# Kernel optimization log

Measured on AMD Instinct MI355X. Metric: run time of the kernel, lower is better.

The kernel has to match this reference:

```python
import jax, jax.numpy as jnp
import numpy as np

N = 100000
E = 1600000
IN_F, HID, OUT_F = 256, 128, 64


def setup_inputs() -> dict:
    key = jax.random.key(0)
    k_x, k_e, k_w1, k_w2, k_b1, k_b2 = jax.random.split(key, 6)
    x = jax.random.normal(k_x, (N, IN_F), dtype=jnp.float32)
    edge_index = jax.random.randint(k_e, (2, E), 0, N, dtype=jnp.int32)
    # GCNConv params: lin has no bias in PyG; separate additive bias per layer.
    W1 = jax.random.normal(k_w1, (IN_F, HID), dtype=jnp.float32) / np.sqrt(IN_F)
    b1 = jax.random.normal(k_b1, (HID,), dtype=jnp.float32) * 0.01
    W2 = jax.random.normal(k_w2, (HID, OUT_F), dtype=jnp.float32) / np.sqrt(HID)
    b2 = jax.random.normal(k_b2, (OUT_F,), dtype=jnp.float32) * 0.01
    return {"x": x, "edge_index": edge_index, "W1": W1, "b1": b1, "W2": W2, "b2": b2}


def _gcn_norm(edge_index, num_nodes):
    # add self loops (improved=False -> weight 1.0), symmetric normalization
    loop = jnp.arange(num_nodes, dtype=edge_index.dtype)
    src = jnp.concatenate([edge_index[0], loop])
    dst = jnp.concatenate([edge_index[1], loop])
    w = jnp.ones(src.shape[0], dtype=jnp.float32)
    deg = jax.ops.segment_sum(w, dst, num_segments=num_nodes)
    dinv = jnp.where(deg > 0, jax.lax.rsqrt(deg), 0.0)
    norm = dinv[src] * w * dinv[dst]
    return src, dst, norm


def _gcn_layer(h, W, b, src, dst, norm, num_nodes):
    h = h @ W                               # [N, out]
    msg = h[src] * norm[:, None]            # [E+N, out] gather + scale
    out = jax.ops.segment_sum(msg, dst, num_segments=num_nodes)  # scatter-add
    return out + b


def reference(x, edge_index, W1, b1, W2, b2):
    # dropout is identity in eval mode
    src, dst, norm = _gcn_norm(edge_index, N)
    h = _gcn_layer(x, W1, b1, src, dst, norm, N)
    h = jax.nn.relu(h)
    out = _gcn_layer(h, W2, b2, src, dst, norm, N)
    return out
```

## Files before the change

### kernel.cpp

```cpp
#include <hip/hip_runtime.h>
#include <hip/hip_bf16.h>

#define N_NODES 100000
#define N_EDGES 1600000
#define IN_FEAT 256
#define HID_F   128
#define OUT_FT  64

#define NBUK   256
#define NPB    391
#define BUKCAP 8192
#define EPB    4096
#define G_BIN  ((N_EDGES + EPB - 1) / EPB)
#define G_GEMM ((N_NODES + 127) / 128)
#define G_CAST ((IN_FEAT * HID_F + HID_F * OUT_FT + 255) / 256)
#define G_AGG  ((N_NODES + 7) / 8)

typedef unsigned short u16;
typedef __attribute__((ext_vector_type(8))) unsigned short u16x8;
typedef __attribute__((ext_vector_type(8))) short short8;
typedef __attribute__((ext_vector_type(4))) float f32x4;

static __device__ inline u16 f2bf(float f) {
    __hip_bfloat16 h = __float2bfloat16(f);
    return *reinterpret_cast<u16*>(&h);
}
static __device__ inline float bf2f(u16 u) {
    union { unsigned u; float f; } c;
    c.u = ((unsigned)u) << 16;
    return c.f;
}


__global__ __launch_bounds__(256) void k_bin(const int* __restrict__ srcA,
                                             const int* __restrict__ dstA,
                                             int* __restrict__ gcur, int2* __restrict__ pairs,
                                             const float* __restrict__ W1,
                                             const float* __restrict__ W2,
                                             u16* __restrict__ W1t, u16* __restrict__ W2t) {
    if (blockIdx.x >= G_BIN) {
        int idx = (blockIdx.x - G_BIN) * 256 + threadIdx.x;
        if (idx < IN_FEAT * HID_F) {
            int k = idx / HID_F, n = idx % HID_F;
            W1t[n * IN_FEAT + k] = f2bf(W1[idx]);
        } else {
            int e2 = idx - IN_FEAT * HID_F;
            if (e2 < HID_F * OUT_FT) {
                int k = e2 / OUT_FT, n = e2 % OUT_FT;
                W2t[n * HID_F + k] = f2bf(W2[e2]);
            }
        }
        return;
    }
    __shared__ int lh[NBUK];
    int t = threadIdx.x;
    int e0 = blockIdx.x * EPB;
    if (t < NBUK) lh[t] = 0;
    __syncthreads();
#pragma unroll
    for (int i = 0; i < EPB / 256; i++) {
        int e = e0 + i * 256 + t;
        if (e < N_EDGES) atomicAdd(&lh[dstA[e] / NPB], 1);
    }
    __syncthreads();
    if (t < NBUK) {
        int c = lh[t];
        lh[t] = atomicAdd(&gcur[t], c);
    }
    __syncthreads();
#pragma unroll
    for (int i = 0; i < EPB / 256; i++) {
        int e = e0 + i * 256 + t;
        if (e < N_EDGES) {
            int d = dstA[e];
            int b = d / NPB;
            int p = atomicAdd(&lh[b], 1);
            if (p < BUKCAP) pairs[(size_t)b * BUKCAP + p] = make_int2(srcA[e], d);
        }
    }
}


__global__ __launch_bounds__(256) void k_fillB(const int2* __restrict__ pairs,
                                               const int* __restrict__ gcnt,
                                               int* __restrict__ offsets,
                                               float* __restrict__ dinv,
                                               int* __restrict__ csr) {
    __shared__ int hist[NPB];
    __shared__ int sm[256];
    __shared__ int s_ebase;
    int b = blockIdx.x, t = threadIdx.x;
    int nbase = b * NPB;
    int nn = min(NPB, N_NODES - nbase);

    int gv = gcnt[t];
    sm[t] = gv;
    __syncthreads();
    for (int o = 1; o < 256; o <<= 1) {
        int u = (t >= o) ? sm[t - o] : 0;
        __syncthreads();
        sm[t] += u;
        __syncthreads();
    }
    if (t == b) s_ebase = sm[t] - gv;
    __syncthreads();
    int ebase = s_ebase;
    int cnt = gcnt[b];
    const int2* pb = pairs + (size_t)b * BUKCAP;

    for (int i = t; i < NPB; i += 256) hist[i] = 0;
    __syncthreads();
    for (int i = t; i < cnt; i += 256) atomicAdd(&hist[pb[i].y - nbase], 1);
    __syncthreads();

    int base2 = t * 2;
    int c0 = (base2 < NPB) ? hist[base2] : 0;
    int c1 = (base2 + 1 < NPB) ? hist[base2 + 1] : 0;
    int s = c0 + c1;
    __syncthreads();
    sm[t] = s;
    __syncthreads();
    for (int o = 1; o < 256; o <<= 1) {
        int u = (t >= o) ? sm[t - o] : 0;
        __syncthreads();
        sm[t] += u;
        __syncthreads();
    }
    int run = ebase + sm[t] - s;
    __syncthreads();
    int cc[2] = {c0, c1};
#pragma unroll
    for (int q = 0; q < 2; q++) {
        int n = base2 + q;
        if (n < nn) {
            int g = nbase + n;
            offsets[g] = run;
            dinv[g] = rsqrtf((float)(cc[q] + 1));
            hist[n] = run;
            run += cc[q];
        }
    }
    __syncthreads();
    for (int i = t; i < cnt; i += 256) {
        int2 e = pb[i];
        int p = atomicAdd(&hist[e.y - nbase], 1);
        csr[p] = e.x;
    }
    if (b == NBUK - 1 && t == 0) offsets[N_NODES] = N_EDGES;
}


__global__ __launch_bounds__(256) void k_gemm1(const float* __restrict__ A,
                                               const u16* __restrict__ Bt,
                                               const float* __restrict__ dinv,
                                               u16* __restrict__ C) {
    __shared__ u16 As[128][40];
    __shared__ u16 Bs[128][40];
    int tid = threadIdx.x;
    int wv = tid >> 6, lane = tid & 63;
    int m16 = lane & 15, quad = lane >> 4;
    int row0 = blockIdx.x * 128;
    int r = tid >> 1, h = tid & 1;
    int grow_s = row0 + r;
    bool rok = grow_s < N_NODES;

    f32x4 acc[2][8];
#pragma unroll
    for (int i = 0; i < 2; i++)
#pragma unroll
        for (int j = 0; j < 8; j++) acc[i][j] = (f32x4)(0.f);

    for (int k0 = 0; k0 < IN_FEAT; k0 += 32) {
        f32x4 v0 = (f32x4)(0.f), v1 = v0, v2 = v0, v3 = v0;
        if (rok) {
            const f32x4* src = (const f32x4*)&A[(size_t)grow_s * IN_FEAT + k0 + h * 16];
            v0 = src[0]; v1 = src[1]; v2 = src[2]; v3 = src[3];
        }
        u16x8 p0, p1;
#pragma unroll
        for (int j = 0; j < 4; j++) {
            p0[j] = f2bf(v0[j]); p0[4 + j] = f2bf(v1[j]);
            p1[j] = f2bf(v2[j]); p1[4 + j] = f2bf(v3[j]);
        }
        *(u16x8*)&As[r][h * 16] = p0;
        *(u16x8*)&As[r][h * 16 + 8] = p1;
        const u16x8* bsrc = (const u16x8*)&Bt[(size_t)r * IN_FEAT + k0 + h * 16];
        *(u16x8*)&Bs[r][h * 16] = bsrc[0];
        *(u16x8*)&Bs[r][h * 16 + 8] = bsrc[1];
        __syncthreads();

        short8 af0 = *(const short8*)&As[32 * wv + m16][quad * 8];
        short8 af1 = *(const short8*)&As[32 * wv + 16 + m16][quad * 8];
#pragma unroll
        for (int ct = 0; ct < 8; ct++) {
            short8 bf = *(const short8*)&Bs[16 * ct + m16][quad * 8];
            acc[0][ct] = __builtin_amdgcn_mfma_f32_16x16x32_bf16(af0, bf, acc[0][ct], 0, 0, 0);
            acc[1][ct] = __builtin_amdgcn_mfma_f32_16x16x32_bf16(af1, bf, acc[1][ct], 0, 0, 0);
        }
        __syncthreads();
    }
#pragma unroll
    for (int rt = 0; rt < 2; rt++)
#pragma unroll
        for (int r4 = 0; r4 < 4; r4++) {
            int grow = row0 + 32 * wv + 16 * rt + quad * 4 + r4;
            if (grow < N_NODES) {
                float dv = dinv[grow];
#pragma unroll
                for (int ct = 0; ct < 8; ct++)
                    C[(size_t)grow * HID_F + 16 * ct + m16] = f2bf(acc[rt][ct][r4] * dv);
            }
        }
}


__global__ __launch_bounds__(256) void k_gemm2(const u16* __restrict__ A,
                                               const u16* __restrict__ Bt,
                                               const float* __restrict__ dinv,
                                               u16* __restrict__ C) {
    __shared__ u16 As[128][40];
    __shared__ u16 Bs[64][40];
    int tid = threadIdx.x;
    int wv = tid >> 6, lane = tid & 63;
    int m16 = lane & 15, quad = lane >> 4;
    int row0 = blockIdx.x * 128;
    int r = tid >> 1, h = tid & 1;
    int grow_s = row0 + r;
    bool rok = grow_s < N_NODES;
    int nb = tid >> 2, q = tid & 3;

    f32x4 acc[2][4];
#pragma unroll
    for (int i = 0; i < 2; i++)
#pragma unroll
        for (int j = 0; j < 4; j++) acc[i][j] = (f32x4)(0.f);

    for (int k0 = 0; k0 < HID_F; k0 += 32) {
        u16x8 a0 = (u16x8)(0), a1v = (u16x8)(0);
        if (rok) {
            const u16x8* src = (const u16x8*)&A[(size_t)grow_s * HID_F + k0 + h * 16];
            a0 = src[0]; a1v = src[1];
        }
        *(u16x8*)&As[r][h * 16] = a0;
        *(u16x8*)&As[r][h * 16 + 8] = a1v;
        *(u16x8*)&Bs[nb][q * 8] = *(const u16x8*)&Bt[(size_t)nb * HID_F + k0 + q * 8];
        __syncthreads();

        short8 af0 = *(const short8*)&As[32 * wv + m16][quad * 8];
        short8 af1 = *(const short8*)&As[32 * wv + 16 + m16][quad * 8];
#pragma unroll
        for (int ct = 0; ct < 4; ct++) {
            short8 bf = *(const short8*)&Bs[16 * ct + m16][quad * 8];
            acc[0][ct] = __builtin_amdgcn_mfma_f32_16x16x32_bf16(af0, bf, acc[0][ct], 0, 0, 0);
            acc[1][ct] = __builtin_amdgcn_mfma_f32_16x16x32_bf16(af1, bf, acc[1][ct], 0, 0, 0);
        }
        __syncthreads();
    }
#pragma unroll
    for (int rt = 0; rt < 2; rt++)
#pragma unroll
        for (int r4 = 0; r4 < 4; r4++) {
            int grow = row0 + 32 * wv + 16 * rt + quad * 4 + r4;
            if (grow < N_NODES) {
                float dv = dinv[grow];
#pragma unroll
                for (int ct = 0; ct < 4; ct++)
                    C[(size_t)grow * OUT_FT + 16 * ct + m16] = f2bf(acc[rt][ct][r4] * dv);
            }
        }
}


__global__ __launch_bounds__(256) void k_agg1(const u16* __restrict__ hs,
                                              const int* __restrict__ offsets,
                                              const int* __restrict__ csr,
                                              const float* __restrict__ dinv,
                                              const float* __restrict__ b,
                                              u16* __restrict__ out) {
    int wave = threadIdx.x >> 6;
    int lane = threadIdx.x & 63;
    int half = lane >> 5;
    int node = blockIdx.x * 8 + wave * 2 + half;
    if (node >= N_NODES) return;
    int gl = lane & 31;
    int g = gl >> 4;
    int fl = gl & 15;
    const int fo = fl * 8;
    int beg = offsets[node], end = offsets[node + 1];

    float accA[8], accB[8];
#pragma unroll
    for (int i = 0; i < 8; i++) { accA[i] = 0.f; accB[i] = 0.f; }

    int j = beg;
    for (; j + 8 <= end; j += 8) {
        int s0 = csr[j + g];
        int s1 = csr[j + 2 + g];
        int s2 = csr[j + 4 + g];
        int s3 = csr[j + 6 + g];
        u16x8 r0 = *(const u16x8*)&hs[(size_t)s0 * HID_F + fo];
        u16x8 r1 = *(const u16x8*)&hs[(size_t)s1 * HID_F + fo];
        u16x8 r2 = *(const u16x8*)&hs[(size_t)s2 * HID_F + fo];
        u16x8 r3 = *(const u16x8*)&hs[(size_t)s3 * HID_F + fo];
#pragma unroll
        for (int i = 0; i < 8; i++) {
            accA[i] += bf2f(r0[i]) + bf2f(r1[i]);
            accB[i] += bf2f(r2[i]) + bf2f(r3[i]);
        }
    }
    if (j + 4 <= end) {
        int s0 = csr[j + g];
        int s1 = csr[j + 2 + g];
        u16x8 r0 = *(const u16x8*)&hs[(size_t)s0 * HID_F + fo];
        u16x8 r1 = *(const u16x8*)&hs[(size_t)s1 * HID_F + fo];
#pragma unroll
        for (int i = 0; i < 8; i++) accA[i] += bf2f(r0[i]) + bf2f(r1[i]);
        j += 4;
    }
    for (; j < end; j += 2) {
        int idx = j + g;
        if (idx < end) {
            int s = csr[idx];
            u16x8 r0 = *(const u16x8*)&hs[(size_t)s * HID_F + fo];
#pragma unroll
            for (int i = 0; i < 8; i++) accB[i] += bf2f(r0[i]);
        }
    }
#pragma unroll
    for (int i = 0; i < 8; i++) {
        float v = accA[i] + accB[i];
        v += __shfl_xor(v, 16, 64);
        accA[i] = v;
    }
    if (g == 0) {
        u16x8 sr = *(const u16x8*)&hs[(size_t)node * HID_F + fo];
        float dv = dinv[node];
        f32x4 b0 = *(const f32x4*)&b[fo];
        f32x4 b1 = *(const f32x4*)&b[fo + 4];
        u16x8 o;
#pragma unroll
        for (int i = 0; i < 4; i++) {
            o[i]     = f2bf(fmaxf(dv * (accA[i]     + bf2f(sr[i]))     + b0[i], 0.f));
            o[4 + i] = f2bf(fmaxf(dv * (accA[4 + i] + bf2f(sr[4 + i])) + b1[i], 0.f));
        }
        *(u16x8*)&out[(size_t)node * HID_F + fo] = o;
    }
}


__global__ __launch_bounds__(256) void k_agg2(const u16* __restrict__ hs,
                                              const int* __restrict__ offsets,
                                              const int* __restrict__ csr,
                                              const float* __restrict__ dinv,
                                              const float* __restrict__ b,
                                              float* __restrict__ out) {
    int wave = threadIdx.x >> 6;
    int lane = threadIdx.x & 63;
    int half = lane >> 5;
    int node = blockIdx.x * 8 + wave * 2 + half;
    if (node >= N_NODES) return;
    int gl = lane & 31;
    int g = gl >> 3;
    int fl = gl & 7;
    const int fo = fl * 8;
    int beg = offsets[node], end = offsets[node + 1];

    float accA[8], accB[8];
#pragma unroll
    for (int i = 0; i < 8; i++) { accA[i] = 0.f; accB[i] = 0.f; }

    int j = beg;
    for (; j + 16 <= end; j += 16) {
        int s0 = csr[j + g];
        int s1 = csr[j + 4 + g];
        int s2 = csr[j + 8 + g];
        int s3 = csr[j + 12 + g];
        u16x8 r0 = *(const u16x8*)&hs[(size_t)s0 * OUT_FT + fo];
        u16x8 r1 = *(const u16x8*)&hs[(size_t)s1 * OUT_FT + fo];
        u16x8 r2 = *(const u16x8*)&hs[(size_t)s2 * OUT_FT + fo];
        u16x8 r3 = *(const u16x8*)&hs[(size_t)s3 * OUT_FT + fo];
#pragma unroll
        for (int i = 0; i < 8; i++) {
            accA[i] += bf2f(r0[i]) + bf2f(r1[i]);
            accB[i] += bf2f(r2[i]) + bf2f(r3[i]);
        }
    }
    if (j + 8 <= end) {
        int s0 = csr[j + g];
        int s1 = csr[j + 4 + g];
        u16x8 r0 = *(const u16x8*)&hs[(size_t)s0 * OUT_FT + fo];
        u16x8 r1 = *(const u16x8*)&hs[(size_t)s1 * OUT_FT + fo];
#pragma unroll
        for (int i = 0; i < 8; i++) accA[i] += bf2f(r0[i]) + bf2f(r1[i]);
        j += 8;
    }
    for (; j < end; j += 4) {
        int idx = j + g;
        if (idx < end) {
            int s = csr[idx];
            u16x8 r0 = *(const u16x8*)&hs[(size_t)s * OUT_FT + fo];
#pragma unroll
            for (int i = 0; i < 8; i++) accB[i] += bf2f(r0[i]);
        }
    }
#pragma unroll
    for (int i = 0; i < 8; i++) {
        float v = accA[i] + accB[i];
        v += __shfl_xor(v, 8, 64);
        v += __shfl_xor(v, 16, 64);
        accA[i] = v;
    }
    if (g == 0) {
        u16x8 sr = *(const u16x8*)&hs[(size_t)node * OUT_FT + fo];
        float dv = dinv[node];
        f32x4 b0 = *(const f32x4*)&b[fo];
        f32x4 b1 = *(const f32x4*)&b[fo + 4];
        f32x4 o0, o1;
#pragma unroll
        for (int i = 0; i < 4; i++) {
            o0[i] = dv * (accA[i]     + bf2f(sr[i]))     + b0[i];
            o1[i] = dv * (accA[4 + i] + bf2f(sr[4 + i])) + b1[i];
        }
        *(f32x4*)&out[(size_t)node * OUT_FT + fo] = o0;
        *(f32x4*)&out[(size_t)node * OUT_FT + fo + 4] = o1;
    }
}


extern "C" void kernel_launch(void* const* d_in, const int* in_sizes, int n_in,
                              void* d_out, int out_size, void* d_ws, size_t ws_size,
                              hipStream_t stream) {
    const float* x  = (const float*)d_in[0];
    const int*   ei = (const int*)d_in[1];
    const float* W1 = (const float*)d_in[2];
    const float* b1 = (const float*)d_in[3];
    const float* W2 = (const float*)d_in[4];
    const float* b2 = (const float*)d_in[5];
    float* out = (float*)d_out;

    char* ws = (char*)d_ws;
    int*   offsets = (int*)(ws + 0);
    float* dinv    = (float*)(ws + 400512);
    int*   csr     = (int*)(ws + 800512);
    u16*   W1t     = (u16*)(ws + 7200512);
    u16*   W2t     = (u16*)(ws + 7266048);
    int*   gcur    = (int*)(ws + 7282432);
    u16*   hs1     = (u16*)(ws + 7284608);
    u16*   a1      = (u16*)(ws + 32884608);
    int2*  pairs   = (int2*)(ws + 32884608);
    u16*   hs2     = hs1;

    const int* srcA = ei;
    const int* dstA = ei + N_EDGES;

    hipMemsetAsync(gcur, 0, NBUK * sizeof(int), stream);

    k_bin<<<G_BIN + G_CAST, 256, 0, stream>>>(srcA, dstA, gcur, pairs, W1, W2, W1t, W2t);
    k_fillB<<<NBUK, 256, 0, stream>>>(pairs, gcur, offsets, dinv, csr);

    k_gemm1<<<G_GEMM, 256, 0, stream>>>(x, W1t, dinv, hs1);
    k_agg1<<<G_AGG, 256, 0, stream>>>(hs1, offsets, csr, dinv, b1, a1);
    k_gemm2<<<G_GEMM, 256, 0, stream>>>(a1, W2t, dinv, hs2);
    k_agg2<<<G_AGG, 256, 0, stream>>>(hs2, offsets, csr, dinv, b2, out);
}
```

Measured before the change: 345.1 us.

## Drop LDS staging in GEMM kernels, load MFMA fragments directly from global

Both dense projection kernels stop staging A and B tiles through shared memory and no longer synchronise the block. Each wave now loads its A fragment and the B fragments straight from global memory into registers. Each wave covers 16 rows instead of 32, so the row tile per block drops to 64 and the grid doubles. This removes LDS traffic and barrier stalls. In exchange, B is re-read from global/L2 by every wave and A loads are strided 32-byte chunks per lane rather than coalesced rows.

Result: slower. 382.6 us (+10.9%).

```diff
diff --git a/kernel.cpp b/kernel.cpp
--- a/kernel.cpp
+++ b/kernel.cpp
@@ -12,7 +12,7 @@
 #define BUKCAP 8192
 #define EPB    4096
 #define G_BIN  ((N_EDGES + EPB - 1) / EPB)
-#define G_GEMM ((N_NODES + 127) / 128)
+#define G_GEMM ((N_NODES + 63) / 64)
 #define G_CAST ((IN_FEAT * HID_F + HID_F * OUT_FT + 255) / 256)
 #define G_AGG  ((N_NODES + 7) / 8)
 
@@ -154,63 +154,44 @@
                                                const u16* __restrict__ Bt,
                                                const float* __restrict__ dinv,
                                                u16* __restrict__ C) {
-    __shared__ u16 As[128][40];
-    __shared__ u16 Bs[128][40];
     int tid = threadIdx.x;
     int wv = tid >> 6, lane = tid & 63;
     int m16 = lane & 15, quad = lane >> 4;
-    int row0 = blockIdx.x * 128;
-    int r = tid >> 1, h = tid & 1;
-    int grow_s = row0 + r;
-    bool rok = grow_s < N_NODES;
-
-    f32x4 acc[2][8];
-#pragma unroll
-    for (int i = 0; i < 2; i++)
-#pragma unroll
-        for (int j = 0; j < 8; j++) acc[i][j] = (f32x4)(0.f);
-
+    int rowbase = blockIdx.x * 64 + wv * 16;
+    int row_a = rowbase + m16;
+    if (row_a >= N_NODES) row_a = N_NODES - 1;
+
+    f32x4 acc[8];
+#pragma unroll
+    for (int j = 0; j < 8; j++) acc[j] = (f32x4)(0.f);
+
+    const float* arow = &A[(size_t)row_a * IN_FEAT + quad * 8];
+
+#pragma unroll 2
     for (int k0 = 0; k0 < IN_FEAT; k0 += 32) {
-        f32x4 v0 = (f32x4)(0.f), v1 = v0, v2 = v0, v3 = v0;
-        if (rok) {
-            const f32x4* src = (const f32x4*)&A[(size_t)grow_s * IN_FEAT + k0 + h * 16];
-            v0 = src[0]; v1 = src[1]; v2 = src[2]; v3 = src[3];
-        }
-        u16x8 p0, p1;
-#pragma unroll
-        for (int j = 0; j < 4; j++) {
-            p0[j] = f2bf(v0[j]); p0[4 + j] = f2bf(v1[j]);
-            p1[j] = f2bf(v2[j]); p1[4 + j] = f2bf(v3[j]);
-        }
-        *(u16x8*)&As[r][h * 16] = p0;
-        *(u16x8*)&As[r][h * 16 + 8] = p1;
-        const u16x8* bsrc = (const u16x8*)&Bt[(size_t)r * IN_FEAT + k0 + h * 16];
-        *(u16x8*)&Bs[r][h * 16] = bsrc[0];
-        *(u16x8*)&Bs[r][h * 16 + 8] = bsrc[1];
-        __syncthreads();
-
-        short8 af0 = *(const short8*)&As[32 * wv + m16][quad * 8];
-        short8 af1 = *(const short8*)&As[32 * wv + 16 + m16][quad * 8];
+        f32x4 a0 = *(const f32x4*)&arow[k0];
+        f32x4 a1 = *(const f32x4*)&arow[k0 + 4];
+        u16x8 af;
+#pragma unroll
+        for (int j = 0; j < 4; j++) { af[j] = f2bf(a0[j]); af[4 + j] = f2bf(a1[j]); }
+        short8 afs = *(short8*)&af;
 #pragma unroll
         for (int ct = 0; ct < 8; ct++) {
-            short8 bf = *(const short8*)&Bs[16 * ct + m16][quad * 8];
-            acc[0][ct] = __builtin_amdgcn_mfma_f32_16x16x32_bf16(af0, bf, acc[0][ct], 0, 0, 0);
-            acc[1][ct] = __builtin_amdgcn_mfma_f32_16x16x32_bf16(af1, bf, acc[1][ct], 0, 0, 0);
-        }
-        __syncthreads();
-    }
-#pragma unroll
-    for (int rt = 0; rt < 2; rt++)
-#pragma unroll
-        for (int r4 = 0; r4 < 4; r4++) {
-            int grow = row0 + 32 * wv + 16 * rt + quad * 4 + r4;
-            if (grow < N_NODES) {
-                float dv = dinv[grow];
-#pragma unroll
-                for (int ct = 0; ct < 8; ct++)
-                    C[(size_t)grow * HID_F + 16 * ct + m16] = f2bf(acc[rt][ct][r4] * dv);
-            }
-        }
+            short8 bf = *(const short8*)&Bt[(size_t)(16 * ct + m16) * IN_FEAT + k0 + quad * 8];
+            acc[ct] = __builtin_amdgcn_mfma_f32_16x16x32_bf16(afs, bf, acc[ct], 0, 0, 0);
+        }
+    }
+
+#pragma unroll
+    for (int r4 = 0; r4 < 4; r4++) {
+        int grow = rowbase + quad * 4 + r4;
+        if (grow < N_NODES) {
+            float dv = dinv[grow];
+#pragma unroll
+            for (int ct = 0; ct < 8; ct++)
+                C[(size_t)grow * HID_F + 16 * ct + m16] = f2bf(acc[ct][r4] * dv);
+        }
+    }
 }
 
 
@@ -218,56 +199,39 @@
                                                const u16* __restrict__ Bt,
                                                const float* __restrict__ dinv,
                                                u16* __restrict__ C) {
-    __shared__ u16 As[128][40];
-    __shared__ u16 Bs[64][40];
     int tid = threadIdx.x;
     int wv = tid >> 6, lane = tid & 63;
     int m16 = lane & 15, quad = lane >> 4;
-    int row0 = blockIdx.x * 128;
-    int r = tid >> 1, h = tid & 1;
-    int grow_s = row0 + r;
-    bool rok = grow_s < N_NODES;
-    int nb = tid >> 2, q = tid & 3;
-
-    f32x4 acc[2][4];
-#pragma unroll
-    for (int i = 0; i < 2; i++)
-#pragma unroll
-        for (int j = 0; j < 4; j++) acc[i][j] = (f32x4)(0.f);
-
+    int rowbase = blockIdx.x * 64 + wv * 16;
+    int row_a = rowbase + m16;
+    if (row_a >= N_NODES) row_a = N_NODES - 1;
+
+    f32x4 acc[4];
+#pragma unroll
+    for (int j = 0; j < 4; j++) acc[j] = (f32x4)(0.f);
+
+    const u16* arow = &A[(size_t)row_a * HID_F + quad * 8];
+
+#pragma unroll
     for (int k0 = 0; k0 < HID_F; k0 += 32) {
-        u16x8 a0 = (u16x8)(0), a1v = (u16x8)(0);
-        if (rok) {
-            const u16x8* src = (const u16x8*)&A[(size_t)grow_s * HID_F + k0 + h * 16];
-            a0 = src[0]; a1v = src[1];
-        }
-        *(u16x8*)&As[r][h * 16] = a0;
-        *(u16x8*)&As[r][h * 16 + 8] = a1v;
-        *(u16x8*)&Bs[nb][q * 8] = *(const u16x8*)&Bt[(size_t)nb * HID_F + k0 + q * 8];
-        __syncthreads();
-
-        short8 af0 = *(const short8*)&As[32 * wv + m16][quad * 8];
-        short8 af1 = *(const short8*)&As[32 * wv + 16 + m16][quad * 8];
+        short8 afs = *(const short8*)&arow[k0];
 #pragma unroll
         for (int ct = 0; ct < 4; ct++) {
-            short8 bf = *(const short8*)&Bs[16 * ct + m16][quad * 8];
-            acc[0][ct] = __builtin_amdgcn_mfma_f32_16x16x32_bf16(af0, bf, acc[0][ct], 0, 0, 0);
-            acc[1][ct] = __builtin_amdgcn_mfma_f32_16x16x32_bf16(af1, bf, acc[1][ct], 0, 0, 0);
-        }
-        __syncthreads();
-    }
-#pragma unroll
-    for (int rt = 0; rt < 2; rt++)
-#pragma unroll
-        for (int r4 = 0; r4 < 4; r4++) {
-            int grow = row0 + 32 * wv + 16 * rt + quad * 4 + r4;
-            if (grow < N_NODES) {
-                float dv = dinv[grow];
-#pragma unroll
-                for (int ct = 0; ct < 4; ct++)
-                    C[(size_t)grow * OUT_FT + 16 * ct + m16] = f2bf(acc[rt][ct][r4] * dv);
-            }
-        }
+            short8 bf = *(const short8*)&Bt[(size_t)(16 * ct + m16) * HID_F + k0 + quad * 8];
+            acc[ct] = __builtin_amdgcn_mfma_f32_16x16x32_bf16(afs, bf, acc[ct], 0, 0, 0);
+        }
+    }
+
+#pragma unroll
+    for (int r4 = 0; r4 < 4; r4++) {
+        int grow = rowbase + quad * 4 + r4;
+        if (grow < N_NODES) {
+            float dv = dinv[grow];
+#pragma unroll
+            for (int ct = 0; ct < 4; ct++)
+                C[(size_t)grow * OUT_FT + 16 * ct + m16] = f2bf(acc[ct][r4] * dv);
+        }
+    }
 }
 
 
```
